# Performance work log

Measured on AMD Instinct MI355X. Metric: run time of the kernel, lower is better.

## Reference

```python
import jax, jax.numpy as jnp
import numpy as np
from jax import lax

CIN, COUT, K, PAD = 256, 128, 3, 1


def setup_inputs() -> dict:
    key = jax.random.key(0)
    ks = jax.random.split(key, 5)
    N, h0, w0 = 2, 64, 64
    x = jax.random.normal(ks[0], (N, CIN, h0, w0), jnp.float32)
    lateral_feat = jax.random.normal(ks[1], (N, COUT, 1, 1), jnp.float32)
    trans_w = jax.random.normal(ks[2], (CIN, COUT, K, K), jnp.float32) * 0.02
    off_w1 = jax.random.normal(ks[3], (64, COUT, 3, 3), jnp.float32) * 0.02
    off_b1 = jnp.zeros((64,), jnp.float32)
    off_w2 = jax.random.normal(ks[4], (2 * K * K, 64, 3, 3), jnp.float32) * 0.02
    off_b2 = jnp.zeros((2 * K * K,), jnp.float32)
    return dict(x=x, lateral_feat=lateral_feat, trans_w=trans_w,
                off_w1=off_w1, off_b1=off_b1, off_w2=off_w2, off_b2=off_b2)


def _conv2d(x, w, b, pad):
    y = lax.conv_general_dilated(x, w, (1, 1), [(pad, pad), (pad, pad)],
                                 dimension_numbers=('NCHW', 'OIHW', 'NCHW'))
    return y + b[None, :, None, None]


def _conv_transpose2d(x, w, stride, pad, out_pad):
    # torch ConvTranspose2d weight layout: [Cin, Cout, k, k]
    k = w.shape[2]
    wt = jnp.flip(w, (2, 3)).transpose(1, 0, 2, 3)  # [Cout, Cin, k, k]
    lo = k - 1 - pad
    hi = k - 1 - pad + out_pad
    return lax.conv_general_dilated(x, wt, (1, 1), [(lo, hi), (lo, hi)],
                                    lhs_dilation=(stride, stride),
                                    dimension_numbers=('NCHW', 'OIHW', 'NCHW'))


def _deform_conv2d(x, offset, w, pad):
    # x [N,C,H,W], offset [N,2*K*K,H,W] (y,x interleaved per kernel tap), w [O,C,K,K]
    N, C, H, W = x.shape
    O = w.shape[0]
    KK = K * K
    off = offset.reshape(N, KK, 2, H, W)
    ky = jnp.arange(KK) // K
    kx = jnp.arange(KK) % K
    py = jnp.arange(H)[None, None, :, None] + (ky - pad)[None, :, None, None] + off[:, :, 0]
    px = jnp.arange(W)[None, None, None, :] + (kx - pad)[None, :, None, None] + off[:, :, 1]
    y0 = jnp.floor(py)
    x0 = jnp.floor(px)
    dy = py - y0
    dx = px - x0
    y0i = y0.astype(jnp.int32)
    x0i = x0.astype(jnp.int32)
    xf = x.reshape(N, C, H * W)

    def corner(yi, xi, wgt):
        valid = (yi >= 0) & (yi < H) & (xi >= 0) & (xi < W)
        idx = (jnp.clip(yi, 0, H - 1) * W + jnp.clip(xi, 0, W - 1)).reshape(N, -1)
        v = jnp.take_along_axis(xf, idx[:, None, :], axis=2).reshape(N, C, KK, H, W)
        return v * (wgt * valid)[:, None]

    sampled = (corner(y0i, x0i, (1 - dy) * (1 - dx))
               + corner(y0i, x0i + 1, (1 - dy) * dx)
               + corner(y0i + 1, x0i, dy * (1 - dx))
               + corner(y0i + 1, x0i + 1, dy * dx))  # [N,C,KK,H,W]
    return jnp.einsum('nckhw,ock->nohw', sampled, w.reshape(O, C, KK))


def reference(x, lateral_feat, trans_w, off_w1, off_b1, off_w2, off_b2):
    up = _conv_transpose2d(x, trans_w, 2, PAD, 1)          # [N, COUT, 2h0, 2w0]
    h = jax.nn.relu(_conv2d(lateral_feat, off_w1, off_b1, 1))
    offset = jnp.tanh(_conv2d(h, off_w2, off_b2, 1))       # [N, 18, 1, 1]
    N, C, H, W = up.shape
    # offset.repeat(1, 1, H, W) with 1x1 spatial input == broadcast to full grid
    offset = jnp.broadcast_to(offset, (N, 2 * K * K, H, W))
    # deform_conv2d uses trans_conv weight [O=CIN, I=COUT, K, K], stride=1, pad=PAD
    return _deform_conv2d(up, offset, trans_w, PAD)        # [N, CIN, H, W]
```

## Files before the change

### kernel.cpp

```cpp
#include <hip/hip_runtime.h>
#include <hip/hip_fp16.h>
#include <math.h>

typedef __attribute__((ext_vector_type(8))) _Float16 f16x8;
typedef __attribute__((ext_vector_type(4))) float f32x4;

__device__ __forceinline__ unsigned short f2h(float f) {
    __half h = __float2half_rn(f);
    union { __half h; unsigned short u; } v; v.h = h; return v.u;
}
__device__ __forceinline__ unsigned pk2h(float lo, float hi) {
    __half2 h = __floats2half2_rn(lo, hi);
    union { __half2 h; unsigned u; } v; v.h = h; return v.u;
}

#define BARRIER() do { asm volatile("s_waitcnt lgkmcnt(0)" ::: "memory"); \
                       __builtin_amdgcn_s_barrier(); } while (0)

__device__ __forceinline__ void blend_store_h(uint4 uA, uint4 uB, uint4 uC, uint4 uD,
                                              __half2 w0, __half2 w1, __half2 w2, __half2 w3,
                                              unsigned short* dst) {
    union U { uint4 u; __half2 h[4]; };
    U a, b, c, d, r;
    a.u = uA; b.u = uB; c.u = uC; d.u = uD;
#pragma unroll
    for (int i = 0; i < 4; ++i)
        r.h[i] = __hfma2(w0, a.h[i], __hfma2(w1, b.h[i], __hfma2(w2, c.h[i], __hmul2(w3, d.h[i]))));
    *(uint4*)dst = r.u;
}

__global__ __launch_bounds__(256) void k_prep(const float* __restrict__ x,
                                              const float* __restrict__ lat,
                                              const float* __restrict__ tw,
                                              const float* __restrict__ w1,
                                              const float* __restrict__ b1,
                                              const float* __restrict__ w2,
                                              const float* __restrict__ b2,
                                              unsigned short* __restrict__ xp,
                                              unsigned short* __restrict__ A2f,
                                              unsigned short* __restrict__ Awf,
                                              int* __restrict__ ipar,
                                              float* __restrict__ fpar) {
    __shared__ float sm[8420];
    int b = blockIdx.x, t = threadIdx.x;
    if (b == 0) {
        for (int i = t; i < 8192; i += 256) sm[(i >> 7) * 129 + (i & 127)] = w1[i * 9 + 4];
        __syncthreads();
        if (t < 128) {
            int n = t >> 6, o = t & 63;
            float s = b1[o];
            const float* ln = lat + n * 128;
#pragma unroll 8
            for (int c = 0; c < 128; ++c) s += ln[c] * sm[o * 129 + c];
            sm[8256 + t] = fmaxf(s, 0.f);
        }
        __syncthreads();
        if (t < 36) {
            int n = t / 18, j = t % 18;
            float s = b2[j];
            for (int o = 0; o < 64; ++o) s += sm[8256 + n * 64 + o] * w2[(j * 64 + o) * 9 + 4];
            float ov = tanhf(s);
            ov = fminf(fmaxf(ov, -0.999999f), 0.999999f);
            sm[8384 + t] = ov;
        }
        __syncthreads();
        if (t < 36) {
            int n = t / 18, j = t % 18;
            int tap = j >> 1, d = j & 1;
            float ov = sm[8384 + t];
            float fl = floorf(ov);
            int kc = d ? (tap % 3) : (tap / 3);
            ipar[(n * 9 + tap) * 2 + d] = kc - 1 + (int)fl;
            fpar[(n * 9 + tap) * 2 + d] = ov - fl;
        }
    } else if (b < 145) {
        int slot = (b - 1) * 256 + t;
        int l = slot & 63;
        int mi = (slot >> 6) & 3;
        int w = (slot >> 8) & 3;
        int k = slot >> 10;
        int row = w * 64 + mi * 16 + (l & 15);
        int kq = l >> 4;
        unsigned short v[8];
#pragma unroll
        for (int j = 0; j < 8; ++j) {
            int kcol = k * 32 + kq * 8 + j;
            int tap = kcol >> 7, c = kcol & 127;
            v[j] = f2h(tw[(row * 128 + c) * 9 + tap]);
        }
        unsigned p0 = (unsigned)v[0] | ((unsigned)v[1] << 16);
        unsigned p1 = (unsigned)v[2] | ((unsigned)v[3] << 16);
        unsigned p2 = (unsigned)v[4] | ((unsigned)v[5] << 16);
        unsigned p3 = (unsigned)v[6] | ((unsigned)v[7] << 16);
        *(uint4*)(A2f + slot * 8) = make_uint4(p0, p1, p2, p3);
    } else if (b < 289) {
        int slot = (b - 145) * 256 + t;
        int l = slot & 63;
        int mi = (slot >> 6) & 3;
        int wm = (slot >> 8) & 1;
        int k = slot >> 9;
        int row = wm * 64 + mi * 16 + (l & 15);
        int kq = l >> 4;
        unsigned short v[8];
#pragma unroll
        for (int j = 0; j < 8; ++j) {
            int kcol = k * 32 + kq * 8 + j;
            int t9 = kcol >> 8, ci = kcol & 255;
            int ky = t9 / 3, kx = t9 - ky * 3;
            v[j] = f2h(tw[(ci * 128 + row) * 9 + (2 - ky) * 3 + (2 - kx)]);
        }
        unsigned p0 = (unsigned)v[0] | ((unsigned)v[1] << 16);
        unsigned p1 = (unsigned)v[2] | ((unsigned)v[3] << 16);
        unsigned p2 = (unsigned)v[4] | ((unsigned)v[5] << 16);
        unsigned p3 = (unsigned)v[6] | ((unsigned)v[7] << 16);
        *(uint4*)(Awf + slot * 8) = make_uint4(p0, p1, p2, p3);
    } else {
        int bb = b - 289;
        int h = bb & 63, cq = (bb >> 6) & 3, n = bb >> 8;
        int c0 = cq * 64;
        {
            int wcol = t & 63, sub = t >> 6;
            for (int r = 0; r < 16; ++r) {
                int ci_l = r * 4 + sub;
                sm[ci_l * 65 + wcol] = x[((n * 256 + c0 + ci_l) * 64 + h) * 64 + wcol];
            }
        }
        __syncthreads();
        int wcol = t >> 2, cg = t & 3;
        unsigned short* dst = xp + (size_t)n * (65 * 65 * 256) + (h * 65 + wcol) * 256 + c0 + cg * 16;
        unsigned pk[8];
#pragma unroll
        for (int j = 0; j < 8; ++j)
            pk[j] = pk2h(sm[(cg * 16 + 2 * j) * 65 + wcol], sm[(cg * 16 + 2 * j + 1) * 65 + wcol]);
        *(uint4*)dst = make_uint4(pk[0], pk[1], pk[2], pk[3]);
        *(uint4*)(dst + 8) = make_uint4(pk[4], pk[5], pk[6], pk[7]);
    }
}

__global__ __launch_bounds__(256) void k_tconv3(const unsigned short* __restrict__ xp,
                                                const unsigned short* __restrict__ Awf,
                                                unsigned short* __restrict__ upp) {
    __shared__ unsigned short Bs[2][2][64][40];
    __shared__ int st9[4];
    __shared__ int sbb[4];
    int t = threadIdx.x;
    int b = blockIdx.x;
    int phase = b & 1;
    int xpar = ((b >> 1) & 1) ^ phase;
    int n = (b >> 2) & 1;
    int yh = b >> 3;
    int y = yh * 2 + phase;
    const unsigned short* xpn = xp + (size_t)n * (65 * 65 * 256);

    int lane = t & 63, w = t >> 6;
    int col = lane & 15, q = lane >> 4;
    int wm = w >> 1, wn = w & 1;
    int bx = t >> 2, bcg = t & 3;
    int boff = bx * 256 + bcg * 8;

    int kys[2], kxs[2], nky, nkx;
    if (phase) { kys[0] = 0; kys[1] = 2; nky = 2; } else { kys[0] = 1; kys[1] = 1; nky = 1; }
    if (xpar)  { kxs[0] = 0; kxs[1] = 2; nkx = 2; } else { kxs[0] = 1; kxs[1] = 1; nkx = 1; }
    int nslots = nky * nkx;
    if (t < 4) {
        int tc = t < nslots ? t : 0;
        int a1 = (nkx == 2) ? (tc >> 1) : tc;
        int a2 = (nkx == 2) ? (tc & 1) : 0;
        int ky = kys[a1], kx = kxs[a2];
        st9[t] = ky * 3 + kx;
        int d2 = (y + ky - 1) >> 1;
        int s = (xpar + kx - 1) >> 1;
        sbb[t] = (d2 * 65 + s) * 256;
    }
    int NPAIR = nslots * 4;

    f32x4 acc[4][2];
#pragma unroll
    for (int mi = 0; mi < 4; ++mi)
#pragma unroll
        for (int ni = 0; ni < 2; ++ni) acc[mi][ni] = (f32x4){0.f, 0.f, 0.f, 0.f};

    __syncthreads();

    const unsigned short* Afw = Awf + wm * 2048 + lane * 8;
    f16x8 aC[2][4], aN[2][4];
    uint4 nb0, nb1;

    {
        int t90 = st9[0], sb0 = sbb[0];
        const unsigned short* pT = xpn + sb0 + boff;
        uint4 b0 = *(const uint4*)pT;
        uint4 b1 = *(const uint4*)(pT + 32);
        const unsigned short* ap = Afw + t90 * 32768;
#pragma unroll
        for (int mi = 0; mi < 4; ++mi) {
            aC[0][mi] = *(const f16x8*)(ap + mi * 512);
            aC[1][mi] = *(const f16x8*)(ap + 4096 + mi * 512);
        }
        *(uint4*)&Bs[0][0][bx][bcg * 8] = b0;
        *(uint4*)&Bs[0][1][bx][bcg * 8] = b1;
    }
    BARRIER();

#define TC_PH(PP, BUF, AC, AN)                                                   \
    {                                                                            \
        int P_ = (PP);                                                           \
        if (P_ + 1 < NPAIR) {                                                    \
            int slot_ = (P_ + 1) >> 2;                                           \
            int cb0_ = ((P_ + 1) & 3) * 2;                                       \
            int t9_ = st9[slot_], sb_ = sbb[slot_];                              \
            const unsigned short* pT_ = xpn + sb_ + boff + cb0_ * 32;            \
            nb0 = *(const uint4*)pT_;                                            \
            nb1 = *(const uint4*)(pT_ + 32);                                     \
            const unsigned short* ap_ = Afw + (t9_ * 8 + cb0_) * 4096;           \
            _Pragma("unroll")                                                    \
            for (int mi = 0; mi < 4; ++mi) {                                     \
                AN[0][mi] = *(const f16x8*)(ap_ + mi * 512);                     \
                AN[1][mi] = *(const f16x8*)(ap_ + 4096 + mi * 512);              \
            }                                                                    \
        }                                                                        \
        f16x8 bb[2][2];                                                          \
        _Pragma("unroll")                                                        \
        for (int c = 0; c < 2; ++c)                                              \
            _Pragma("unroll")                                                    \
            for (int ni = 0; ni < 2; ++ni)                                       \
                bb[c][ni] = *(const f16x8*)&Bs[BUF][c][wn * 32 + ni * 16 + col][q * 8]; \
        _Pragma("unroll")                                                        \
        for (int c = 0; c < 2; ++c)                                              \
            _Pragma("unroll")                                                    \
            for (int mi = 0; mi < 4; ++mi)                                       \
                _Pragma("unroll")                                                \
                for (int ni = 0; ni < 2; ++ni)                                   \
                    acc[mi][ni] = __builtin_amdgcn_mfma_f32_16x16x32_f16(AC[c][mi], bb[c][ni], acc[mi][ni], 0, 0, 0); \
        if (P_ + 1 < NPAIR) {                                                    \
            *(uint4*)&Bs[BUF ^ 1][0][bx][bcg * 8] = nb0;                         \
            *(uint4*)&Bs[BUF ^ 1][1][bx][bcg * 8] = nb1;                         \
        }                                                                        \
        BARRIER();                                                               \
    }

    for (int pp = 0; pp < NPAIR; pp += 2) {
        TC_PH(pp,     0, aC, aN);
        TC_PH(pp + 1, 1, aN, aC);
    }
#undef TC_PH

    unsigned short* uppn = upp + (size_t)n * (132 * 132 * 128);
#pragma unroll
    for (int mi = 0; mi < 4; ++mi)
#pragma unroll
        for (int ni = 0; ni < 2; ++ni) {
            int co = wm * 64 + mi * 16 + q * 4;
            int p64 = wn * 32 + ni * 16 + col;
            int xg = 2 * p64 + xpar;
            unsigned short* p = uppn + ((y + 2) * 132 + (xg + 2)) * 128 + co;
            unsigned lo = pk2h(acc[mi][ni][0], acc[mi][ni][1]);
            unsigned hi = pk2h(acc[mi][ni][2], acc[mi][ni][3]);
            *(uint2*)p = make_uint2(lo, hi);
        }
}

__global__ __launch_bounds__(256) void k_deform3(const unsigned short* __restrict__ upp,
                                                 const unsigned short* __restrict__ A2f,
                                                 const int* __restrict__ ipar,
                                                 const float* __restrict__ fpar,
                                                 float* __restrict__ out) {
    __shared__ unsigned short Bs[2][2][64][40];
    __shared__ int sbase[9];
    __shared__ __half2 swh[9][4];
    int t = threadIdx.x;
    int b = blockIdx.x;
    int xcd = b & 7, j = b >> 3;
    int n = xcd >> 2, band = xcd & 3;
    int y = band * 32 + (j & 31);
    int tx0 = (j >> 5) * 64;
    const unsigned short* uppn = upp + (size_t)n * (132 * 132 * 128);

    int lane = t & 63, w = t >> 6;
    int col = lane & 15, q = lane >> 4;
    int bx = t >> 2, bcg = t & 3;
    int boff = bx * 128 + bcg * 8;

    if (t < 9) {
        int iy = ipar[(n * 9 + t) * 2 + 0], ix = ipar[(n * 9 + t) * 2 + 1];
        float fy = fpar[(n * 9 + t) * 2 + 0], fx = fpar[(n * 9 + t) * 2 + 1];
        sbase[t] = ((y + 2 + iy) * 132 + (tx0 + 2 + ix)) * 128;
        swh[t][0] = __float2half2_rn((1.f - fy) * (1.f - fx));
        swh[t][1] = __float2half2_rn((1.f - fy) * fx);
        swh[t][2] = __float2half2_rn(fy * (1.f - fx));
        swh[t][3] = __float2half2_rn(fy * fx);
    }

    f32x4 acc[4][4];
#pragma unroll
    for (int mi = 0; mi < 4; ++mi)
#pragma unroll
        for (int ni = 0; ni < 4; ++ni) acc[mi][ni] = (f32x4){0.f, 0.f, 0.f, 0.f};

    __syncthreads();

    const unsigned short* Afw = A2f + w * 2048 + lane * 8;
    f16x8 aC[2][4], aN[2][4];
    uint4 cA0, cB0, cC0, cD0, cA1, cB1, cC1, cD1;

    {
        const unsigned short* pAt = uppn + sbase[0] + boff;
        const unsigned short* pCt = pAt + 16896;
        __half2 w0 = swh[0][0], w1 = swh[0][1], w2 = swh[0][2], w3 = swh[0][3];
        uint4 uA0 = *(const uint4*)pAt;
        uint4 uB0 = *(const uint4*)(pAt + 128);
        uint4 uC0 = *(const uint4*)pCt;
        uint4 uD0 = *(const uint4*)(pCt + 128);
        uint4 uA1 = *(const uint4*)(pAt + 32);
        uint4 uB1 = *(const uint4*)(pAt + 160);
        uint4 uC1 = *(const uint4*)(pCt + 32);
        uint4 uD1 = *(const uint4*)(pCt + 160);
#pragma unroll
        for (int mi = 0; mi < 4; ++mi) {
            aC[0][mi] = *(const f16x8*)(Afw + mi * 512);
            aC[1][mi] = *(const f16x8*)(Afw + 8192 + mi * 512);
        }
        blend_store_h(uA0, uB0, uC0, uD0, w0, w1, w2, w3, &Bs[0][0][bx][bcg * 8]);
        blend_store_h(uA1, uB1, uC1, uD1, w0, w1, w2, w3, &Bs[0][1][bx][bcg * 8]);
    }
    BARRIER();

#define DEF_PH(PP, BUF, AC, AN)                                                  \
    {                                                                            \
        int P_ = (PP);                                                           \
        __half2 w0_, w1_, w2_, w3_;                                              \
        if (P_ + 1 < 18) {                                                       \
            int tap_ = (P_ + 1) >> 1;                                            \
            int sh_ = ((P_ + 1) & 1) * 64;                                       \
            int sb_ = sbase[tap_];                                               \
            w0_ = swh[tap_][0]; w1_ = swh[tap_][1];                              \
            w2_ = swh[tap_][2]; w3_ = swh[tap_][3];                              \
            const unsigned short* pAt_ = uppn + sb_ + boff + sh_;                \
            const unsigned short* pCt_ = pAt_ + 16896;                           \
            cA0 = *(const uint4*)pAt_;                                           \
            cB0 = *(const uint4*)(pAt_ + 128);                                   \
            cC0 = *(const uint4*)pCt_;                                           \
            cD0 = *(const uint4*)(pCt_ + 128);                                   \
            cA1 = *(const uint4*)(pAt_ + 32);                                    \
            cB1 = *(const uint4*)(pAt_ + 160);                                   \
            cC1 = *(const uint4*)(pCt_ + 32);                                    \
            cD1 = *(const uint4*)(pCt_ + 160);                                   \
            const unsigned short* ap_ = Afw + (P_ + 1) * 16384;                  \
            _Pragma("unroll")                                                    \
            for (int mi = 0; mi < 4; ++mi) {                                     \
                AN[0][mi] = *(const f16x8*)(ap_ + mi * 512);                     \
                AN[1][mi] = *(const f16x8*)(ap_ + 8192 + mi * 512);              \
            }                                                                    \
        }                                                                        \
        f16x8 bb[2][4];                                                          \
        _Pragma("unroll")                                                        \
        for (int c = 0; c < 2; ++c)                                              \
            _Pragma("unroll")                                                    \
            for (int ni = 0; ni < 4; ++ni)                                       \
                bb[c][ni] = *(const f16x8*)&Bs[BUF][c][ni * 16 + col][q * 8];    \
        _Pragma("unroll")                                                        \
        for (int c = 0; c < 2; ++c)                                              \
            _Pragma("unroll")                                                    \
            for (int mi = 0; mi < 4; ++mi)                                       \
                _Pragma("unroll")                                                \
                for (int ni = 0; ni < 4; ++ni)                                   \
                    acc[mi][ni] = __builtin_amdgcn_mfma_f32_16x16x32_f16(AC[c][mi], bb[c][ni], acc[mi][ni], 0, 0, 0); \
        if (P_ + 1 < 18) {                                                       \
            blend_store_h(cA0, cB0, cC0, cD0, w0_, w1_, w2_, w3_, &Bs[BUF ^ 1][0][bx][bcg * 8]); \
            blend_store_h(cA1, cB1, cC1, cD1, w0_, w1_, w2_, w3_, &Bs[BUF ^ 1][1][bx][bcg * 8]); \
        }                                                                        \
        BARRIER();                                                               \
    }

    for (int pp = 0; pp < 18; pp += 2) {
        DEF_PH(pp,     0, aC, aN);
        DEF_PH(pp + 1, 1, aN, aC);
    }
#undef DEF_PH

#pragma unroll
    for (int mi = 0; mi < 4; ++mi)
#pragma unroll
        for (int ni = 0; ni < 4; ++ni) {
            int o = w * 64 + mi * 16 + q * 4;
            int xg = tx0 + ni * 16 + col;
            float* p = out + (((size_t)(n * 256 + o)) * 128 + y) * 128 + xg;
            p[0]         = acc[mi][ni][0];
            p[16384]     = acc[mi][ni][1];
            p[2 * 16384] = acc[mi][ni][2];
            p[3 * 16384] = acc[mi][ni][3];
        }
}

extern "C" void kernel_launch(void* const* d_in, const int* in_sizes, int n_in,
                              void* d_out, int out_size, void* d_ws, size_t ws_size,
                              hipStream_t stream) {
    const float* x   = (const float*)d_in[0];
    const float* lat = (const float*)d_in[1];
    const float* tw  = (const float*)d_in[2];
    const float* w1  = (const float*)d_in[3];
    const float* b1  = (const float*)d_in[4];
    const float* w2  = (const float*)d_in[5];
    const float* b2  = (const float*)d_in[6];
    float* out = (float*)d_out;

    char* ws = (char*)d_ws;
    unsigned short* upp = (unsigned short*)ws;
    unsigned short* xp  = (unsigned short*)(ws + 8921088);
    unsigned short* A2f = (unsigned short*)(ws + 13247488);
    unsigned short* Awf = (unsigned short*)(ws + 13837312);
    int*   ipar         = (int*)(ws + 14427136);
    float* fpar         = (float*)(ws + 14427424);

    hipMemsetAsync(ws, 0, 13247488, stream);
    k_prep<<<801, 256, 0, stream>>>(x, lat, tw, w1, b1, w2, b2, xp, A2f, Awf, ipar, fpar);
    k_tconv3<<<512, 256, 0, stream>>>(xp, Awf, upp);
    k_deform3<<<512, 256, 0, stream>>>(upp, A2f, ipar, fpar, out);
}
```

Before: 139.1 us.

## Batch both images per tconv block and zero only upp borders in prep

The transposed-conv kernel now covers both batch images in one block, so each block loads a given set of A (weight) fragments once and applies them to twice as many B columns. The grid is halved and the accumulator tile doubles. The full-workspace memset is replaced by zeroing only the padded xp region, and extra k_prep blocks write zeros to the 2-pixel border of upp. This cuts weight reload traffic and memset bandwidth, at the cost of higher register pressure and fewer blocks in the GEMM kernel.

Result: no change. 140.6 us (+1.1%).

```diff
diff --git a/kernel.cpp b/kernel.cpp
--- a/kernel.cpp
+++ b/kernel.cpp
@@ -39,6 +39,7 @@
                                               unsigned short* __restrict__ xp,
                                               unsigned short* __restrict__ A2f,
                                               unsigned short* __restrict__ Awf,
+                                              unsigned short* __restrict__ upp,
                                               int* __restrict__ ipar,
                                               float* __restrict__ fpar) {
     __shared__ float sm[8420];
@@ -114,7 +115,7 @@
         unsigned p2 = (unsigned)v[4] | ((unsigned)v[5] << 16);
         unsigned p3 = (unsigned)v[6] | ((unsigned)v[7] << 16);
         *(uint4*)(Awf + slot * 8) = make_uint4(p0, p1, p2, p3);
-    } else {
+    } else if (b < 801) {
         int bb = b - 289;
         int h = bb & 63, cq = (bb >> 6) & 3, n = bb >> 8;
         int c0 = cq * 64;
@@ -134,29 +135,46 @@
             pk[j] = pk2h(sm[(cg * 16 + 2 * j) * 65 + wcol], sm[(cg * 16 + 2 * j + 1) * 65 + wcol]);
         *(uint4*)dst = make_uint4(pk[0], pk[1], pk[2], pk[3]);
         *(uint4*)(dst + 8) = make_uint4(pk[4], pk[5], pk[6], pk[7]);
+    } else {
+        int g = (b - 801) * 256 + t;
+        int n2 = g >= 16640 ? 1 : 0;
+        int i = g - n2 * 16640;
+        int px_id = i >> 4, chv = i & 15;
+        int r, c;
+        if (px_id < 528) {
+            int rr = px_id / 132;
+            r = rr < 2 ? rr : 128 + rr;
+            c = px_id - rr * 132;
+        } else {
+            int jj = px_id - 528;
+            r = 2 + (jj >> 2);
+            int cc = jj & 3;
+            c = cc < 2 ? cc : 128 + cc;
+        }
+        uint4* p = (uint4*)(upp + (size_t)n2 * (132 * 132 * 128) + ((r * 132 + c) * 128) + chv * 8);
+        *p = make_uint4(0u, 0u, 0u, 0u);
     }
 }
 
 __global__ __launch_bounds__(256) void k_tconv3(const unsigned short* __restrict__ xp,
                                                 const unsigned short* __restrict__ Awf,
                                                 unsigned short* __restrict__ upp) {
-    __shared__ unsigned short Bs[2][2][64][40];
+    __shared__ unsigned short Bs[2][2][128][40];
     __shared__ int st9[4];
     __shared__ int sbb[4];
     int t = threadIdx.x;
     int b = blockIdx.x;
     int phase = b & 1;
     int xpar = ((b >> 1) & 1) ^ phase;
-    int n = (b >> 2) & 1;
-    int yh = b >> 3;
+    int yh = b >> 2;
     int y = yh * 2 + phase;
-    const unsigned short* xpn = xp + (size_t)n * (65 * 65 * 256);
 
     int lane = t & 63, w = t >> 6;
     int col = lane & 15, q = lane >> 4;
     int wm = w >> 1, wn = w & 1;
-    int bx = t >> 2, bcg = t & 3;
-    int boff = bx * 256 + bcg * 8;
+    int bx2 = t >> 1, bcg2 = t & 1;
+    int spx = bx2 & 63, snn = bx2 >> 6;
+    const unsigned short* xpt = xp + (size_t)snn * (65 * 65 * 256) + spx * 256 + bcg2 * 16;
 
     int kys[2], kxs[2], nky, nkx;
     if (phase) { kys[0] = 0; kys[1] = 2; nky = 2; } else { kys[0] = 1; kys[1] = 1; nky = 1; }
@@ -174,31 +192,34 @@
     }
     int NPAIR = nslots * 4;
 
-    f32x4 acc[4][2];
+    f32x4 acc[4][4];
 #pragma unroll
     for (int mi = 0; mi < 4; ++mi)
 #pragma unroll
-        for (int ni = 0; ni < 2; ++ni) acc[mi][ni] = (f32x4){0.f, 0.f, 0.f, 0.f};
+        for (int ni = 0; ni < 4; ++ni) acc[mi][ni] = (f32x4){0.f, 0.f, 0.f, 0.f};
 
     __syncthreads();
 
     const unsigned short* Afw = Awf + wm * 2048 + lane * 8;
     f16x8 aC[2][4], aN[2][4];
-    uint4 nb0, nb1;
+    uint4 nb0, nb1, nb2, nb3;
 
     {
-        int t90 = st9[0], sb0 = sbb[0];
-        const unsigned short* pT = xpn + sb0 + boff;
-        uint4 b0 = *(const uint4*)pT;
-        uint4 b1 = *(const uint4*)(pT + 32);
-        const unsigned short* ap = Afw + t90 * 32768;
+        const unsigned short* p0 = xpt + sbb[0];
+        uint4 b00 = *(const uint4*)p0;
+        uint4 b01 = *(const uint4*)(p0 + 8);
+        uint4 b10 = *(const uint4*)(p0 + 32);
+        uint4 b11 = *(const uint4*)(p0 + 40);
+        const unsigned short* ap = Afw + st9[0] * 32768;
 #pragma unroll
         for (int mi = 0; mi < 4; ++mi) {
             aC[0][mi] = *(const f16x8*)(ap + mi * 512);
             aC[1][mi] = *(const f16x8*)(ap + 4096 + mi * 512);
         }
-        *(uint4*)&Bs[0][0][bx][bcg * 8] = b0;
-        *(uint4*)&Bs[0][1][bx][bcg * 8] = b1;
+        *(uint4*)&Bs[0][0][bx2][bcg2 * 16]     = b00;
+        *(uint4*)&Bs[0][0][bx2][bcg2 * 16 + 8] = b01;
+        *(uint4*)&Bs[0][1][bx2][bcg2 * 16]     = b10;
+        *(uint4*)&Bs[0][1][bx2][bcg2 * 16 + 8] = b11;
     }
     BARRIER();
 
@@ -208,33 +229,36 @@
         if (P_ + 1 < NPAIR) {                                                    \
             int slot_ = (P_ + 1) >> 2;                                           \
             int cb0_ = ((P_ + 1) & 3) * 2;                                       \
-            int t9_ = st9[slot_], sb_ = sbb[slot_];                              \
-            const unsigned short* pT_ = xpn + sb_ + boff + cb0_ * 32;            \
+            const unsigned short* pT_ = xpt + sbb[slot_] + cb0_ * 32;            \
             nb0 = *(const uint4*)pT_;                                            \
-            nb1 = *(const uint4*)(pT_ + 32);                                     \
-            const unsigned short* ap_ = Afw + (t9_ * 8 + cb0_) * 4096;           \
+            nb1 = *(const uint4*)(pT_ + 8);                                      \
+            nb2 = *(const uint4*)(pT_ + 32);                                     \
+            nb3 = *(const uint4*)(pT_ + 40);                                     \
+            const unsigned short* ap_ = Afw + (st9[slot_] * 8 + cb0_) * 4096;    \
             _Pragma("unroll")                                                    \
             for (int mi = 0; mi < 4; ++mi) {                                     \
                 AN[0][mi] = *(const f16x8*)(ap_ + mi * 512);                     \
                 AN[1][mi] = *(const f16x8*)(ap_ + 4096 + mi * 512);              \
             }                                                                    \
         }                                                                        \
-        f16x8 bb[2][2];                                                          \
+        f16x8 bb[2][4];                                                          \
         _Pragma("unroll")                                                        \
         for (int c = 0; c < 2; ++c)                                              \
             _Pragma("unroll")                                                    \
-            for (int ni = 0; ni < 2; ++ni)                                       \
-                bb[c][ni] = *(const f16x8*)&Bs[BUF][c][wn * 32 + ni * 16 + col][q * 8]; \
+            for (int ni = 0; ni < 4; ++ni)                                       \
+                bb[c][ni] = *(const f16x8*)&Bs[BUF][c][wn * 64 + ni * 16 + col][q * 8]; \
         _Pragma("unroll")                                                        \
         for (int c = 0; c < 2; ++c)                                              \
             _Pragma("unroll")                                                    \
             for (int mi = 0; mi < 4; ++mi)                                       \
                 _Pragma("unroll")                                                \
-                for (int ni = 0; ni < 2; ++ni)                                   \
+                for (int ni = 0; ni < 4; ++ni)                                   \
                     acc[mi][ni] = __builtin_amdgcn_mfma_f32_16x16x32_f16(AC[c][mi], bb[c][ni], acc[mi][ni], 0, 0, 0); \
         if (P_ + 1 < NPAIR) {                                                    \
-            *(uint4*)&Bs[BUF ^ 1][0][bx][bcg * 8] = nb0;                         \
-            *(uint4*)&Bs[BUF ^ 1][1][bx][bcg * 8] = nb1;                         \
+            *(uint4*)&Bs[BUF ^ 1][0][bx2][bcg2 * 16]     = nb0;                  \
+            *(uint4*)&Bs[BUF ^ 1][0][bx2][bcg2 * 16 + 8] = nb1;                  \
+            *(uint4*)&Bs[BUF ^ 1][1][bx2][bcg2 * 16]     = nb2;                  \
+            *(uint4*)&Bs[BUF ^ 1][1][bx2][bcg2 * 16 + 8] = nb3;                  \
         }                                                                        \
         BARRIER();                                                               \
     }
@@ -245,13 +269,13 @@
     }
 #undef TC_PH
 
-    unsigned short* uppn = upp + (size_t)n * (132 * 132 * 128);
+    unsigned short* uppn = upp + (size_t)wn * (132 * 132 * 128);
 #pragma unroll
     for (int mi = 0; mi < 4; ++mi)
 #pragma unroll
-        for (int ni = 0; ni < 2; ++ni) {
+        for (int ni = 0; ni < 4; ++ni) {
             int co = wm * 64 + mi * 16 + q * 4;
-            int p64 = wn * 32 + ni * 16 + col;
+            int p64 = ni * 16 + col;
             int xg = 2 * p64 + xpar;
             unsigned short* p = uppn + ((y + 2) * 132 + (xg + 2)) * 128 + co;
             unsigned lo = pk2h(acc[mi][ni][0], acc[mi][ni][1]);
@@ -412,8 +436,8 @@
     int*   ipar         = (int*)(ws + 14427136);
     float* fpar         = (float*)(ws + 14427424);
 
-    hipMemsetAsync(ws, 0, 13247488, stream);
-    k_prep<<<801, 256, 0, stream>>>(x, lat, tw, w1, b1, w2, b2, xp, A2f, Awf, ipar, fpar);
-    k_tconv3<<<512, 256, 0, stream>>>(xp, Awf, upp);
+    hipMemsetAsync(ws + 8921088, 0, 4326400, stream);
+    k_prep<<<931, 256, 0, stream>>>(x, lat, tw, w1, b1, w2, b2, xp, A2f, Awf, upp, ipar, fpar);
+    k_tconv3<<<256, 256, 0, stream>>>(xp, Awf, upp);
     k_deform3<<<512, 256, 0, stream>>>(upp, A2f, ipar, fpar, out);
 }
```

## Zero only upp border in prep kernel and raise MFMA wave priority

Applied to the files above, without the earlier changes.

The full workspace memset no longer covers the padded upsampled buffer. Its 2-pixel border ring is now zeroed by 130 extra blocks in k_prep, and the memset is restricted to the xp region, cutting about 9 MB of redundant zero writes. Both GEMM kernels also wrap their MFMA loops in s_setprio(1)/s_setprio(0) so waves issuing matrix ops are favoured by the scheduler. The border-zeroing assumes the interior is fully overwritten by k_tconv3.

New measurement: 147.0 us. +5.7%, slower.

```diff
diff --git a/kernel.cpp b/kernel.cpp
--- a/kernel.cpp
+++ b/kernel.cpp
@@ -39,6 +39,7 @@
                                               unsigned short* __restrict__ xp,
                                               unsigned short* __restrict__ A2f,
                                               unsigned short* __restrict__ Awf,
+                                              unsigned short* __restrict__ upp,
                                               int* __restrict__ ipar,
                                               float* __restrict__ fpar) {
     __shared__ float sm[8420];
@@ -114,7 +115,7 @@
         unsigned p2 = (unsigned)v[4] | ((unsigned)v[5] << 16);
         unsigned p3 = (unsigned)v[6] | ((unsigned)v[7] << 16);
         *(uint4*)(Awf + slot * 8) = make_uint4(p0, p1, p2, p3);
-    } else {
+    } else if (b < 801) {
         int bb = b - 289;
         int h = bb & 63, cq = (bb >> 6) & 3, n = bb >> 8;
         int c0 = cq * 64;
@@ -134,6 +135,24 @@
             pk[j] = pk2h(sm[(cg * 16 + 2 * j) * 65 + wcol], sm[(cg * 16 + 2 * j + 1) * 65 + wcol]);
         *(uint4*)dst = make_uint4(pk[0], pk[1], pk[2], pk[3]);
         *(uint4*)(dst + 8) = make_uint4(pk[4], pk[5], pk[6], pk[7]);
+    } else {
+        int g = (b - 801) * 256 + t;
+        int n2 = g >= 16640 ? 1 : 0;
+        int i = g - n2 * 16640;
+        int px_id = i >> 4, chv = i & 15;
+        int r, c;
+        if (px_id < 528) {
+            int rr = px_id / 132;
+            r = rr < 2 ? rr : 128 + rr;
+            c = px_id - rr * 132;
+        } else {
+            int jj = px_id - 528;
+            r = 2 + (jj >> 2);
+            int cc = jj & 3;
+            c = cc < 2 ? cc : 128 + cc;
+        }
+        uint4* p = (uint4*)(upp + (size_t)n2 * (132 * 132 * 128) + ((r * 132 + c) * 128) + chv * 8);
+        *p = make_uint4(0u, 0u, 0u, 0u);
     }
 }
 
@@ -187,11 +206,10 @@
     uint4 nb0, nb1;
 
     {
-        int t90 = st9[0], sb0 = sbb[0];
-        const unsigned short* pT = xpn + sb0 + boff;
+        const unsigned short* pT = xpn + sbb[0] + boff;
         uint4 b0 = *(const uint4*)pT;
         uint4 b1 = *(const uint4*)(pT + 32);
-        const unsigned short* ap = Afw + t90 * 32768;
+        const unsigned short* ap = Afw + st9[0] * 32768;
 #pragma unroll
         for (int mi = 0; mi < 4; ++mi) {
             aC[0][mi] = *(const f16x8*)(ap + mi * 512);
@@ -208,11 +226,10 @@
         if (P_ + 1 < NPAIR) {                                                    \
             int slot_ = (P_ + 1) >> 2;                                           \
             int cb0_ = ((P_ + 1) & 3) * 2;                                       \
-            int t9_ = st9[slot_], sb_ = sbb[slot_];                              \
-            const unsigned short* pT_ = xpn + sb_ + boff + cb0_ * 32;            \
+            const unsigned short* pT_ = xpn + sbb[slot_] + cb0_ * 32 + boff;     \
             nb0 = *(const uint4*)pT_;                                            \
             nb1 = *(const uint4*)(pT_ + 32);                                     \
-            const unsigned short* ap_ = Afw + (t9_ * 8 + cb0_) * 4096;           \
+            const unsigned short* ap_ = Afw + (st9[slot_] * 8 + cb0_) * 4096;    \
             _Pragma("unroll")                                                    \
             for (int mi = 0; mi < 4; ++mi) {                                     \
                 AN[0][mi] = *(const f16x8*)(ap_ + mi * 512);                     \
@@ -225,6 +242,7 @@
             _Pragma("unroll")                                                    \
             for (int ni = 0; ni < 2; ++ni)                                       \
                 bb[c][ni] = *(const f16x8*)&Bs[BUF][c][wn * 32 + ni * 16 + col][q * 8]; \
+        __builtin_amdgcn_s_setprio(1);                                           \
         _Pragma("unroll")                                                        \
         for (int c = 0; c < 2; ++c)                                              \
             _Pragma("unroll")                                                    \
@@ -232,6 +250,7 @@
                 _Pragma("unroll")                                                \
                 for (int ni = 0; ni < 2; ++ni)                                   \
                     acc[mi][ni] = __builtin_amdgcn_mfma_f32_16x16x32_f16(AC[c][mi], bb[c][ni], acc[mi][ni], 0, 0, 0); \
+        __builtin_amdgcn_s_setprio(0);                                           \
         if (P_ + 1 < NPAIR) {                                                    \
             *(uint4*)&Bs[BUF ^ 1][0][bx][bcg * 8] = nb0;                         \
             *(uint4*)&Bs[BUF ^ 1][1][bx][bcg * 8] = nb1;                         \
@@ -358,6 +377,7 @@
             _Pragma("unroll")                                                    \
             for (int ni = 0; ni < 4; ++ni)                                       \
                 bb[c][ni] = *(const f16x8*)&Bs[BUF][c][ni * 16 + col][q * 8];    \
+        __builtin_amdgcn_s_setprio(1);                                           \
         _Pragma("unroll")                                                        \
         for (int c = 0; c < 2; ++c)                                              \
             _Pragma("unroll")                                                    \
@@ -365,6 +385,7 @@
                 _Pragma("unroll")                                                \
                 for (int ni = 0; ni < 4; ++ni)                                   \
                     acc[mi][ni] = __builtin_amdgcn_mfma_f32_16x16x32_f16(AC[c][mi], bb[c][ni], acc[mi][ni], 0, 0, 0); \
+        __builtin_amdgcn_s_setprio(0);                                           \
         if (P_ + 1 < 18) {                                                       \
             blend_store_h(cA0, cB0, cC0, cD0, w0_, w1_, w2_, w3_, &Bs[BUF ^ 1][0][bx][bcg * 8]); \
             blend_store_h(cA1, cB1, cC1, cD1, w0_, w1_, w2_, w3_, &Bs[BUF ^ 1][1][bx][bcg * 8]); \
@@ -412,8 +433,8 @@
     int*   ipar         = (int*)(ws + 14427136);
     float* fpar         = (float*)(ws + 14427424);
 
-    hipMemsetAsync(ws, 0, 13247488, stream);
-    k_prep<<<801, 256, 0, stream>>>(x, lat, tw, w1, b1, w2, b2, xp, A2f, Awf, ipar, fpar);
+    hipMemsetAsync(ws + 8921088, 0, 4326400, stream);
+    k_prep<<<931, 256, 0, stream>>>(x, lat, tw, w1, b1, w2, b2, xp, A2f, Awf, upp, ipar, fpar);
     k_tconv3<<<512, 256, 0, stream>>>(xp, Awf, upp);
     k_deform3<<<512, 256, 0, stream>>>(upp, A2f, ipar, fpar, out);
 }
```
